# Kernel tuning notes

Hardware: AMD Instinct MI355X
Metric: run time of the kernel (lower is better)

## Reference

```python
import jax, jax.numpy as jnp
import numpy as np

NIN = 4096
NOUT = 4096
LN_EPS = 1e-5  # torch.nn.LayerNorm default


def setup_inputs() -> dict:
    key = jax.random.key(0)
    ks = jax.random.split(key, 8)
    x = jax.random.normal(ks[0], (1, NIN), dtype=jnp.float32)
    hid = jax.random.normal(ks[1], (1, NOUT), dtype=jnp.float32)
    hebb = jnp.zeros((NOUT, NOUT), dtype=jnp.float32) + 1e-6  # initialZeroHebb
    # parameters
    w_in = 0.01 * jax.random.normal(ks[2], (NOUT, NIN), dtype=jnp.float32)  # inp_lin weight (no bias)
    w = 0.01 * jnp.eye(NOUT, NOUT, dtype=jnp.float32)                        # Plastic.w
    alpha = 0.01 * jax.random.normal(ks[3], (NOUT, NOUT), dtype=jnp.float32)
    b = 0.01 * jax.random.normal(ks[4], (NOUT,), dtype=jnp.float32)
    lamda = 0.01 * jnp.ones((1,), dtype=jnp.float32)
    pred_eta = 0.01 * jax.random.normal(ks[5], (NOUT, NOUT), dtype=jnp.float32)
    pred_eta_b = 0.01 * jax.random.normal(ks[6], (NOUT,), dtype=jnp.float32)
    ln_gamma = jnp.ones((NOUT,), dtype=jnp.float32)
    ln_beta = jnp.zeros((NOUT,), dtype=jnp.float32)
    return {"x": x, "hid": hid, "hebb": hebb, "w_in": w_in, "w": w,
            "alpha": alpha, "b": b, "lamda": lamda, "pred_eta": pred_eta,
            "pred_eta_b": pred_eta_b, "ln_gamma": ln_gamma, "ln_beta": ln_beta}


def reference(x, hid, hebb, w_in, w, alpha, b, lamda, pred_eta, pred_eta_b, ln_gamma, ln_beta):
    # Cell.forward (nonlin = ReLU for both wx and the post-LN output)
    wx = jax.nn.relu(x @ w_in.T)                       # [1, nout]
    wh = hid @ (w + alpha * hebb) + b                  # Plastic.forward, [1, nout]
    s = wx + wh
    mu = jnp.mean(s, axis=-1, keepdims=True)
    var = jnp.mean((s - mu) ** 2, axis=-1, keepdims=True)
    ln = ln_gamma * (s - mu) * jax.lax.rsqrt(var + LN_EPS) + ln_beta
    wy = jax.nn.relu(ln)                               # new hidden state, [1, nout]
    # Plastic.update_hebb(x=hid, y=wh, hebb)
    eta_hat = jax.nn.sigmoid(wh @ pred_eta + pred_eta_b)           # [1, nout]
    outer = hid[0, :, None] * wh[0, None, :]                        # [nout, nout]
    hebb_new = (1.0 - lamda) * hebb + eta_hat.T * outer             # row i scaled by eta_hat[0, i]
    return wy, hebb_new
```

## Files before the change

### kernel.cpp

```cpp
#include <hip/hip_runtime.h>
#include <hip/hip_bf16.h>
#include <math.h>

#define N 4096
#define NGRP 16

typedef float f32x4 __attribute__((ext_vector_type(4)));

__inline__ __device__ float waveReduceSum(float v) {
    #pragma unroll
    for (int o = 32; o > 0; o >>= 1) v += __shfl_down(v, o);
    return v;
}

#define LD4(p, o) (*reinterpret_cast<const float4*>((p) + (o)))

__inline__ __device__ f32x4 ntld4(const float* p) {
    return __builtin_nontemporal_load(reinterpret_cast<const f32x4*>(p));
}

template<int ITERS>
__global__ __launch_bounds__(256) void k_sweep_wh_t(const float* __restrict__ hid,
                                                    const float* __restrict__ w,
                                                    const float* __restrict__ alpha,
                                                    const float* __restrict__ hebb,
                                                    float* __restrict__ part,
                                                    int G) {
    int b = blockIdx.x, t = threadIdx.x;
    int p = b >> 2;
    int j0 = (((b & 3) << 8) | t) * 4;
    int P = G >> 2;
    size_t step = (size_t)G * 1024;
    size_t off = (size_t)(((b << 8) | t)) * 4;

    f32x4 wv[ITERS], av[ITERS], bv[ITERS];
    float hv[ITERS];
    #pragma unroll
    for (int k = 0; k < ITERS; ++k) {
        size_t o = off + (size_t)k * step;
        wv[k] = ntld4(w + o);
        av[k] = ntld4(alpha + o);
        bv[k] = *reinterpret_cast<const f32x4*>(hebb + o);
    }
    #pragma unroll
    for (int k = 0; k < ITERS; ++k) hv[k] = hid[k * P + p];

    f32x4 acc = {0.f, 0.f, 0.f, 0.f};
    #pragma unroll
    for (int k = 0; k < ITERS; ++k) {
        float h = hv[k];
        acc.x = fmaf(h, fmaf(av[k].x, bv[k].x, wv[k].x), acc.x);
        acc.y = fmaf(h, fmaf(av[k].y, bv[k].y, wv[k].y), acc.y);
        acc.z = fmaf(h, fmaf(av[k].z, bv[k].z, wv[k].z), acc.z);
        acc.w = fmaf(h, fmaf(av[k].w, bv[k].w, wv[k].w), acc.w);
    }
    *reinterpret_cast<f32x4*>(part + (size_t)p * N + j0) = acc;
}

__global__ __launch_bounds__(256) void k_sweep_wh(const float* __restrict__ hid,
                                                  const float* __restrict__ w,
                                                  const float* __restrict__ alpha,
                                                  const float* __restrict__ hebb,
                                                  float* __restrict__ part,
                                                  int G, int iters) {
    int b = blockIdx.x, t = threadIdx.x;
    int p = b >> 2;
    int j0 = (((b & 3) << 8) | t) * 4;
    int P = G >> 2;
    float4 acc = make_float4(0.f, 0.f, 0.f, 0.f);
    size_t step = (size_t)G * 1024;
    size_t off = (size_t)(((b << 8) | t)) * 4;
    #pragma unroll 8
    for (int k = 0; k < iters; ++k, off += step) {
        float h = hid[k * P + p];
        float4 wv = LD4(w, off);
        float4 av = LD4(alpha, off);
        float4 hv = LD4(hebb, off);
        acc.x = fmaf(h, fmaf(av.x, hv.x, wv.x), acc.x);
        acc.y = fmaf(h, fmaf(av.y, hv.y, wv.y), acc.y);
        acc.z = fmaf(h, fmaf(av.z, hv.z, wv.z), acc.z);
        acc.w = fmaf(h, fmaf(av.w, hv.w, wv.w), acc.w);
    }
    *reinterpret_cast<float4*>(part + (size_t)p * N + j0) = acc;
}

template<int ITERS>
__global__ __launch_bounds__(256) void k_sweep_eta_t(const float* __restrict__ wh,
                                                     const float* __restrict__ pe,
                                                     float* __restrict__ part,
                                                     int G) {
    int b = blockIdx.x, t = threadIdx.x;
    int p = b >> 2;
    int j0 = (((b & 3) << 8) | t) * 4;
    int P = G >> 2;
    size_t step = (size_t)G * 1024;
    size_t off = (size_t)(((b << 8) | t)) * 4;

    f32x4 pv[ITERS];
    float hv[ITERS];
    #pragma unroll
    for (int k = 0; k < ITERS; ++k) pv[k] = *reinterpret_cast<const f32x4*>(pe + off + (size_t)k * step);
    #pragma unroll
    for (int k = 0; k < ITERS; ++k) hv[k] = wh[k * P + p];

    f32x4 acc = {0.f, 0.f, 0.f, 0.f};
    #pragma unroll
    for (int k = 0; k < ITERS; ++k) {
        float h = hv[k];
        acc.x = fmaf(h, pv[k].x, acc.x);
        acc.y = fmaf(h, pv[k].y, acc.y);
        acc.z = fmaf(h, pv[k].z, acc.z);
        acc.w = fmaf(h, pv[k].w, acc.w);
    }
    *reinterpret_cast<f32x4*>(part + (size_t)p * N + j0) = acc;
}

__global__ __launch_bounds__(256) void k_sweep_eta(const float* __restrict__ wh,
                                                   const float* __restrict__ pe,
                                                   float* __restrict__ part,
                                                   int G, int iters) {
    int b = blockIdx.x, t = threadIdx.x;
    int p = b >> 2;
    int j0 = (((b & 3) << 8) | t) * 4;
    int P = G >> 2;
    float4 acc = make_float4(0.f, 0.f, 0.f, 0.f);
    size_t step = (size_t)G * 1024;
    size_t off = (size_t)(((b << 8) | t)) * 4;
    #pragma unroll 8
    for (int k = 0; k < iters; ++k, off += step) {
        float h = wh[k * P + p];
        float4 pv = LD4(pe, off);
        acc.x = fmaf(h, pv.x, acc.x);
        acc.y = fmaf(h, pv.y, acc.y);
        acc.z = fmaf(h, pv.z, acc.z);
        acc.w = fmaf(h, pv.w, acc.w);
    }
    *reinterpret_cast<float4*>(part + (size_t)p * N + j0) = acc;
}

__global__ __launch_bounds__(256) void k_red_wx(const float* __restrict__ part,
                                                float* __restrict__ part2,
                                                int cpg,
                                                const float* __restrict__ x,
                                                const float* __restrict__ w_in,
                                                float* __restrict__ wx_out,
                                                int nred) {
    int t = threadIdx.x;
    if ((int)blockIdx.x < nred) {
        int g  = blockIdx.x >> 2;
        int xt = blockIdx.x & 3;
        int j0 = (xt * 256 + t) * 4;
        const float4* p4 = reinterpret_cast<const float4*>(part);
        float4 s = make_float4(0.f, 0.f, 0.f, 0.f);
        #pragma unroll 8
        for (int c = 0; c < cpg; ++c) {
            float4 v = p4[((size_t)(g * cpg + c) * N + j0) >> 2];
            s.x += v.x; s.y += v.y; s.z += v.z; s.w += v.w;
        }
        *reinterpret_cast<float4*>(part2 + (size_t)g * N + j0) = s;
    } else {
        int j = blockIdx.x - nred;
        const float4* row = reinterpret_cast<const float4*>(w_in + (size_t)j * N);
        const float4* xv  = reinterpret_cast<const float4*>(x);
        float sum = 0.f;
        #pragma unroll
        for (int k = t; k < N / 4; k += 256) {
            float4 a = row[k], c = xv[k];
            sum += a.x * c.x + a.y * c.y + a.z * c.z + a.w * c.w;
        }
        sum = waveReduceSum(sum);
        __shared__ float wsum[4];
        int wid = t >> 6, lane = t & 63;
        if (lane == 0) wsum[wid] = sum;
        __syncthreads();
        if (t == 0)
            wx_out[j] = fmaxf(wsum[0] + wsum[1] + wsum[2] + wsum[3], 0.f);
    }
}

__global__ __launch_bounds__(1024) void k_ln(const float* __restrict__ part2,
                                             const float* __restrict__ wx,
                                             const float* __restrict__ b,
                                             const float* __restrict__ gamma,
                                             const float* __restrict__ beta,
                                             float* __restrict__ wh_out,
                                             float* __restrict__ wy_out) {
    __shared__ float red[16];
    __shared__ float bc[2];
    int tid = threadIdx.x;
    int wid = tid >> 6, lane = tid & 63;
    float sv[4];
    float lsum = 0.f;
    #pragma unroll
    for (int q = 0; q < 4; ++q) {
        int j = q * 1024 + tid;
        float acc = b[j];
        #pragma unroll
        for (int g = 0; g < NGRP; ++g) acc += part2[(size_t)g * N + j];
        wh_out[j] = acc;
        float s = acc + wx[j];
        sv[q] = s;
        lsum += s;
    }
    float wv = waveReduceSum(lsum);
    if (lane == 0) red[wid] = wv;
    __syncthreads();
    if (tid < 64) {
        float t = (tid < 16) ? red[tid] : 0.f;
        t = waveReduceSum(t);
        if (tid == 0) bc[0] = t * (1.f / N);
    }
    __syncthreads();
    float mean = bc[0];
    __syncthreads();
    float lsq = 0.f;
    #pragma unroll
    for (int q = 0; q < 4; ++q) { float d = sv[q] - mean; lsq += d * d; }
    wv = waveReduceSum(lsq);
    if (lane == 0) red[wid] = wv;
    __syncthreads();
    if (tid < 64) {
        float t = (tid < 16) ? red[tid] : 0.f;
        t = waveReduceSum(t);
        if (tid == 0) bc[1] = t * (1.f / N);
    }
    __syncthreads();
    float rstd = rsqrtf(bc[1] + 1e-5f);
    #pragma unroll
    for (int q = 0; q < 4; ++q) {
        int j = q * 1024 + tid;
        float ln = fmaf(gamma[j] * (sv[q] - mean), rstd, beta[j]);
        wy_out[j] = fmaxf(ln, 0.f);
    }
}

__global__ __launch_bounds__(1024) void k_redfin_hebb(const float* __restrict__ part,
                                                      const float* __restrict__ pb,
                                                      const float* __restrict__ wh,
                                                      const float* __restrict__ hid,
                                                      const float* __restrict__ lamda,
                                                      const float* __restrict__ hebb,
                                                      float* __restrict__ out,
                                                      int P) {
    __shared__ float sm[64][17];
    __shared__ float coef_s[16];
    int t  = threadIdx.x;
    int i0 = blockIdx.x * 16;
    int il = t & 15;
    int ps = t >> 4;
    int q  = P >> 6;

    float s = 0.f;
    for (int k = 0; k < q; ++k)
        s += part[(size_t)(ps * q + k) * N + i0 + il];
    sm[ps][il] = s;
    __syncthreads();
    #pragma unroll
    for (int off = 32; off >= 1; off >>= 1) {
        if (ps < off) sm[ps][il] += sm[ps + off][il];
        __syncthreads();
    }
    if (t < 16) {
        int i = i0 + t;
        float eta = 1.f / (1.f + expf(-(sm[0][t] + pb[i])));
        coef_s[t] = eta * hid[i];
    }
    __syncthreads();

    float decay = 1.f - lamda[0];
    int j = t * 4;
    float4 w4 = LD4(wh, j);
    size_t base = (size_t)i0 * N + j;
    #pragma unroll 4
    for (int r = 0; r < 16; ++r) {
        float coef = coef_s[r];
        float4 h = LD4(hebb, base + (size_t)r * N);
        f32x4 o;
        o.x = fmaf(decay, h.x, coef * w4.x);
        o.y = fmaf(decay, h.y, coef * w4.y);
        o.z = fmaf(decay, h.z, coef * w4.z);
        o.w = fmaf(decay, h.w, coef * w4.w);
        __builtin_nontemporal_store(o, reinterpret_cast<f32x4*>(out + base + (size_t)r * N));
    }
}

extern "C" void kernel_launch(void* const* d_in, const int* in_sizes, int n_in,
                              void* d_out, int out_size, void* d_ws, size_t ws_size,
                              hipStream_t stream) {
    const float* x         = (const float*)d_in[0];
    const float* hid       = (const float*)d_in[1];
    const float* hebb      = (const float*)d_in[2];
    const float* w_in      = (const float*)d_in[3];
    const float* w         = (const float*)d_in[4];
    const float* alpha     = (const float*)d_in[5];
    const float* b         = (const float*)d_in[6];
    const float* lamda     = (const float*)d_in[7];
    const float* pred_eta  = (const float*)d_in[8];
    const float* pred_eta_b= (const float*)d_in[9];
    const float* ln_gamma  = (const float*)d_in[10];
    const float* ln_beta   = (const float*)d_in[11];

    float* wy       = (float*)d_out;
    float* hebb_out = (float*)d_out + N;

    int G = 2048;
    if ((ws_size / 4) < ((size_t)(G / 4) * N + (NGRP + 2) * (size_t)N)) G = 512;
    int P = G / 4;
    int cpg = P / NGRP;
    int iters = (N * (N / 4)) / (G * 256);
    int nred = 4 * NGRP;

    float* ws    = (float*)d_ws;
    float* part  = ws;
    float* part2 = part + (size_t)P * N;
    float* wx    = part2 + (size_t)NGRP * N;
    float* wh    = wx + N;

    if (G == 2048) {
        k_sweep_wh_t<8><<<G, 256, 0, stream>>>(hid, w, alpha, hebb, part, G);
    } else {
        k_sweep_wh<<<G, 256, 0, stream>>>(hid, w, alpha, hebb, part, G, iters);
    }
    k_red_wx<<<nred + N, 256, 0, stream>>>(part, part2, cpg, x, w_in, wx, nred);
    k_ln    <<<1, 1024, 0, stream>>>(part2, wx, b, ln_gamma, ln_beta, wh, wy);
    if (G == 2048) {
        k_sweep_eta_t<8><<<G, 256, 0, stream>>>(wh, pred_eta, part, G);
    } else {
        k_sweep_eta<<<G, 256, 0, stream>>>(wh, pred_eta, part, G, iters);
    }
    k_redfin_hebb<<<256, 1024, 0, stream>>>(part, pred_eta_b, wh, hid, lamda, hebb, hebb_out, P);
}
```

Before: 97.28 us.

## Fuse five-kernel pipeline into one cooperative persistent kernel with grid syncs

Replaces the five-launch sequence (wh sweep, reduce+wx, layernorm, eta sweep, reduce+hebb update) with a single cooperative kernel of 1024 blocks that separates phases with grid.sync(). The wx GEMV is folded into the first phase, and the final reduction now writes per-row coefficients before a separate hebb update phase. This is meant to remove launch gaps and inter-kernel drains. In exchange it adds grid-wide barriers, halves the grid size so each block sweeps 16 rows, and runs the layernorm serially on a single block while the rest of the grid waits. It falls back to the old path if cooperative launch is unavailable or occupancy is too low, and the fallback drops the small-workspace G=512 variant.

```diff
diff --git a/kernel.cpp b/kernel.cpp
--- a/kernel.cpp
+++ b/kernel.cpp
@@ -1,10 +1,13 @@
 #include <hip/hip_runtime.h>
+#include <hip/hip_cooperative_groups.h>
 #include <hip/hip_bf16.h>
 #include <math.h>
 
 #define N 4096
 #define NGRP 16
 
+namespace cg = cooperative_groups;
+
 typedef float f32x4 __attribute__((ext_vector_type(4)));
 
 __inline__ __device__ float waveReduceSum(float v) {
@@ -17,6 +20,207 @@
 
 __inline__ __device__ f32x4 ntld4(const float* p) {
     return __builtin_nontemporal_load(reinterpret_cast<const f32x4*>(p));
+}
+
+template<int ITERS>
+__global__ __launch_bounds__(256, 4) void k_coop(
+    const float* __restrict__ x, const float* __restrict__ hid,
+    const float* __restrict__ hebb, const float* __restrict__ w_in,
+    const float* __restrict__ w, const float* __restrict__ alpha,
+    const float* __restrict__ bvec, const float* __restrict__ lamda,
+    const float* __restrict__ pe, const float* __restrict__ pb,
+    const float* __restrict__ gamma, const float* __restrict__ beta,
+    float* __restrict__ part, float* __restrict__ part2,
+    float* __restrict__ wxv, float* __restrict__ whv,
+    float* __restrict__ coef, float* __restrict__ wy,
+    float* __restrict__ hebb_out, int G)
+{
+    cg::grid_group grid = cg::this_grid();
+    const int b = blockIdx.x, t = threadIdx.x;
+    const int P = G >> 2;
+    const int lane = t & 63, wid = t >> 6;
+    __shared__ float sm[16][17];
+    __shared__ float smb[4];
+    __shared__ float bc[2];
+
+    {
+        int p = b >> 2;
+        int j0 = (((b & 3) << 8) | t) * 4;
+        size_t step = (size_t)G * 1024;
+        size_t off = (size_t)(((b << 8) | t)) * 4;
+        f32x4 acc = {0.f, 0.f, 0.f, 0.f};
+        #pragma unroll
+        for (int h8 = 0; h8 < ITERS / 8; ++h8) {
+            f32x4 wv[8], av[8], bv[8];
+            float hv[8];
+            #pragma unroll
+            for (int k = 0; k < 8; ++k) {
+                size_t o = off + (size_t)(h8 * 8 + k) * step;
+                wv[k] = ntld4(w + o);
+                av[k] = ntld4(alpha + o);
+                bv[k] = *reinterpret_cast<const f32x4*>(hebb + o);
+            }
+            #pragma unroll
+            for (int k = 0; k < 8; ++k) hv[k] = hid[(h8 * 8 + k) * P + p];
+            #pragma unroll
+            for (int k = 0; k < 8; ++k) {
+                float h = hv[k];
+                acc.x = fmaf(h, fmaf(av[k].x, bv[k].x, wv[k].x), acc.x);
+                acc.y = fmaf(h, fmaf(av[k].y, bv[k].y, wv[k].y), acc.y);
+                acc.z = fmaf(h, fmaf(av[k].z, bv[k].z, wv[k].z), acc.z);
+                acc.w = fmaf(h, fmaf(av[k].w, bv[k].w, wv[k].w), acc.w);
+            }
+        }
+        *reinterpret_cast<f32x4*>(part + (size_t)p * N + j0) = acc;
+    }
+    {
+        int rpb = N / G;
+        const float4* xv = reinterpret_cast<const float4*>(x);
+        for (int r = 0; r < rpb; ++r) {
+            int j = b * rpb + r;
+            const float4* row = reinterpret_cast<const float4*>(w_in + (size_t)j * N);
+            float sum = 0.f;
+            #pragma unroll
+            for (int c = 0; c < 4; ++c) {
+                int k = t + c * 256;
+                float4 a = row[k], xc = xv[k];
+                sum += a.x * xc.x + a.y * xc.y + a.z * xc.z + a.w * xc.w;
+            }
+            sum = waveReduceSum(sum);
+            if (lane == 0) smb[wid] = sum;
+            __syncthreads();
+            if (t == 0) wxv[j] = fmaxf(smb[0] + smb[1] + smb[2] + smb[3], 0.f);
+            __syncthreads();
+        }
+    }
+    grid.sync();
+
+    if (b < 4 * NGRP) {
+        int g = b >> 2, xt = b & 3;
+        int j0 = (xt * 256 + t) * 4;
+        int cpg = P / NGRP;
+        const f32x4* p4 = reinterpret_cast<const f32x4*>(part);
+        f32x4 s = {0.f, 0.f, 0.f, 0.f};
+        for (int c = 0; c < cpg; ++c) {
+            f32x4 v = p4[((size_t)(g * cpg + c) * N + j0) >> 2];
+            s.x += v.x; s.y += v.y; s.z += v.z; s.w += v.w;
+        }
+        *reinterpret_cast<f32x4*>(part2 + (size_t)g * N + j0) = s;
+    }
+    grid.sync();
+
+    if (b == 0) {
+        float sv[16];
+        float lsum = 0.f;
+        #pragma unroll
+        for (int q = 0; q < 16; ++q) {
+            int j = q * 256 + t;
+            float acc = bvec[j];
+            #pragma unroll
+            for (int g = 0; g < NGRP; ++g) acc += part2[(size_t)g * N + j];
+            whv[j] = acc;
+            float s = acc + wxv[j];
+            sv[q] = s;
+            lsum += s;
+        }
+        float wr = waveReduceSum(lsum);
+        if (lane == 0) smb[wid] = wr;
+        __syncthreads();
+        if (t == 0) bc[0] = (smb[0] + smb[1] + smb[2] + smb[3]) * (1.f / N);
+        __syncthreads();
+        float mean = bc[0];
+        float lsq = 0.f;
+        #pragma unroll
+        for (int q = 0; q < 16; ++q) { float d = sv[q] - mean; lsq += d * d; }
+        float wr2 = waveReduceSum(lsq);
+        if (lane == 0) smb[wid] = wr2;
+        __syncthreads();
+        if (t == 0) bc[1] = (smb[0] + smb[1] + smb[2] + smb[3]) * (1.f / N);
+        __syncthreads();
+        float rstd = rsqrtf(bc[1] + 1e-5f);
+        #pragma unroll
+        for (int q = 0; q < 16; ++q) {
+            int j = q * 256 + t;
+            float ln = fmaf(gamma[j] * (sv[q] - mean), rstd, beta[j]);
+            wy[j] = fmaxf(ln, 0.f);
+        }
+    }
+    grid.sync();
+
+    {
+        int p = b >> 2;
+        int j0 = (((b & 3) << 8) | t) * 4;
+        size_t step = (size_t)G * 1024;
+        size_t off = (size_t)(((b << 8) | t)) * 4;
+        f32x4 acc = {0.f, 0.f, 0.f, 0.f};
+        #pragma unroll
+        for (int h8 = 0; h8 < ITERS / 8; ++h8) {
+            f32x4 pv[8];
+            float hv[8];
+            #pragma unroll
+            for (int k = 0; k < 8; ++k)
+                pv[k] = *reinterpret_cast<const f32x4*>(pe + off + (size_t)(h8 * 8 + k) * step);
+            #pragma unroll
+            for (int k = 0; k < 8; ++k) hv[k] = whv[(h8 * 8 + k) * P + p];
+            #pragma unroll
+            for (int k = 0; k < 8; ++k) {
+                float h = hv[k];
+                acc.x = fmaf(h, pv[k].x, acc.x);
+                acc.y = fmaf(h, pv[k].y, acc.y);
+                acc.z = fmaf(h, pv[k].z, acc.z);
+                acc.w = fmaf(h, pv[k].w, acc.w);
+            }
+        }
+        *reinterpret_cast<f32x4*>(part + (size_t)p * N + j0) = acc;
+    }
+    grid.sync();
+
+    if (b < 256) {
+        int i0 = b * 16;
+        int il = t & 15, ps = t >> 4;
+        int q2 = P >> 4;
+        float s = 0.f;
+        for (int k = 0; k < q2; ++k)
+            s += part[(size_t)(ps * q2 + k) * N + i0 + il];
+        sm[ps][il] = s;
+        __syncthreads();
+        #pragma unroll
+        for (int off2 = 8; off2 >= 1; off2 >>= 1) {
+            if (ps < off2) sm[ps][il] += sm[ps + off2][il];
+            __syncthreads();
+        }
+        if (t < 16) {
+            int i = i0 + t;
+            float eta = 1.f / (1.f + expf(-(sm[0][t] + pb[i])));
+            coef[i] = eta * hid[i];
+        }
+    }
+    grid.sync();
+
+    {
+        float decay = 1.f - lamda[0];
+        int rpb = N / G;
+        for (int r = 0; r < rpb; ++r) {
+            int i = b * rpb + r;
+            float cf = coef[i];
+            size_t base = (size_t)i * N;
+            const f32x4* hrow = reinterpret_cast<const f32x4*>(hebb + base);
+            f32x4* orow = reinterpret_cast<f32x4*>(hebb_out + base);
+            const f32x4* wrow = reinterpret_cast<const f32x4*>(whv);
+            #pragma unroll
+            for (int c = 0; c < 4; ++c) {
+                int k = t + c * 256;
+                f32x4 h = hrow[k];
+                f32x4 wv4 = wrow[k];
+                f32x4 o;
+                o.x = fmaf(decay, h.x, cf * wv4.x);
+                o.y = fmaf(decay, h.y, cf * wv4.y);
+                o.z = fmaf(decay, h.z, cf * wv4.z);
+                o.w = fmaf(decay, h.w, cf * wv4.w);
+                __builtin_nontemporal_store(o, orow + k);
+            }
+        }
+    }
 }
 
 template<int ITERS>
@@ -32,7 +236,6 @@
     int P = G >> 2;
     size_t step = (size_t)G * 1024;
     size_t off = (size_t)(((b << 8) | t)) * 4;
-
     f32x4 wv[ITERS], av[ITERS], bv[ITERS];
     float hv[ITERS];
     #pragma unroll
@@ -44,7 +247,6 @@
     }
     #pragma unroll
     for (int k = 0; k < ITERS; ++k) hv[k] = hid[k * P + p];
-
     f32x4 acc = {0.f, 0.f, 0.f, 0.f};
     #pragma unroll
     for (int k = 0; k < ITERS; ++k) {
@@ -55,33 +257,6 @@
         acc.w = fmaf(h, fmaf(av[k].w, bv[k].w, wv[k].w), acc.w);
     }
     *reinterpret_cast<f32x4*>(part + (size_t)p * N + j0) = acc;
-}
-
-__global__ __launch_bounds__(256) void k_sweep_wh(const float* __restrict__ hid,
-                                                  const float* __restrict__ w,
-                                                  const float* __restrict__ alpha,
-                                                  const float* __restrict__ hebb,
-                                                  float* __restrict__ part,
-                                                  int G, int iters) {
-    int b = blockIdx.x, t = threadIdx.x;
-    int p = b >> 2;
-    int j0 = (((b & 3) << 8) | t) * 4;
-    int P = G >> 2;
-    float4 acc = make_float4(0.f, 0.f, 0.f, 0.f);
-    size_t step = (size_t)G * 1024;
-    size_t off = (size_t)(((b << 8) | t)) * 4;
-    #pragma unroll 8
-    for (int k = 0; k < iters; ++k, off += step) {
-        float h = hid[k * P + p];
-        float4 wv = LD4(w, off);
-        float4 av = LD4(alpha, off);
-        float4 hv = LD4(hebb, off);
-        acc.x = fmaf(h, fmaf(av.x, hv.x, wv.x), acc.x);
-        acc.y = fmaf(h, fmaf(av.y, hv.y, wv.y), acc.y);
-        acc.z = fmaf(h, fmaf(av.z, hv.z, wv.z), acc.z);
-        acc.w = fmaf(h, fmaf(av.w, hv.w, wv.w), acc.w);
-    }
-    *reinterpret_cast<float4*>(part + (size_t)p * N + j0) = acc;
 }
 
 template<int ITERS>
@@ -95,14 +270,12 @@
     int P = G >> 2;
     size_t step = (size_t)G * 1024;
     size_t off = (size_t)(((b << 8) | t)) * 4;
-
     f32x4 pv[ITERS];
     float hv[ITERS];
     #pragma unroll
     for (int k = 0; k < ITERS; ++k) pv[k] = *reinterpret_cast<const f32x4*>(pe + off + (size_t)k * step);
     #pragma unroll
     for (int k = 0; k < ITERS; ++k) hv[k] = wh[k * P + p];
-
     f32x4 acc = {0.f, 0.f, 0.f, 0.f};
     #pragma unroll
     for (int k = 0; k < ITERS; ++k) {
@@ -113,29 +286,6 @@
         acc.w = fmaf(h, pv[k].w, acc.w);
     }
     *reinterpret_cast<f32x4*>(part + (size_t)p * N + j0) = acc;
-}
-
-__global__ __launch_bounds__(256) void k_sweep_eta(const float* __restrict__ wh,
-                                                   const float* __restrict__ pe,
-                                                   float* __restrict__ part,
-                                                   int G, int iters) {
-    int b = blockIdx.x, t = threadIdx.x;
-    int p = b >> 2;
-    int j0 = (((b & 3) << 8) | t) * 4;
-    int P = G >> 2;
-    float4 acc = make_float4(0.f, 0.f, 0.f, 0.f);
-    size_t step = (size_t)G * 1024;
-    size_t off = (size_t)(((b << 8) | t)) * 4;
-    #pragma unroll 8
-    for (int k = 0; k < iters; ++k, off += step) {
-        float h = wh[k * P + p];
-        float4 pv = LD4(pe, off);
-        acc.x = fmaf(h, pv.x, acc.x);
-        acc.y = fmaf(h, pv.y, acc.y);
-        acc.z = fmaf(h, pv.z, acc.z);
-        acc.w = fmaf(h, pv.w, acc.w);
-    }
-    *reinterpret_cast<float4*>(part + (size_t)p * N + j0) = acc;
 }
 
 __global__ __launch_bounds__(256) void k_red_wx(const float* __restrict__ part,
@@ -293,7 +443,7 @@
     const float* w_in      = (const float*)d_in[3];
     const float* w         = (const float*)d_in[4];
     const float* alpha     = (const float*)d_in[5];
-    const float* b         = (const float*)d_in[6];
+    const float* bvec      = (const float*)d_in[6];
     const float* lamda     = (const float*)d_in[7];
     const float* pred_eta  = (const float*)d_in[8];
     const float* pred_eta_b= (const float*)d_in[9];
@@ -303,30 +453,52 @@
     float* wy       = (float*)d_out;
     float* hebb_out = (float*)d_out + N;
 
+    const int Gc = 1024;
+    const int Pc = Gc / 4;
+    bool wsOK = (ws_size / 4) >= ((size_t)Pc * N + (size_t)(NGRP + 3) * N);
+
+    int dev = 0;
+    hipGetDevice(&dev);
+    int coopAttr = 0, numCU = 0;
+    hipDeviceGetAttribute(&coopAttr, hipDeviceAttributeCooperativeLaunch, dev);
+    hipDeviceGetAttribute(&numCU, hipDeviceAttributeMultiprocessorCount, dev);
+    int maxB = 0;
+    hipOccupancyMaxActiveBlocksPerMultiprocessor(&maxB, (const void*)&k_coop<16>, 256, 0);
+
+    if (coopAttr && wsOK && maxB > 0 && (size_t)maxB * (size_t)numCU >= (size_t)Gc) {
+        float* ws    = (float*)d_ws;
+        float* part  = ws;
+        float* part2 = part + (size_t)Pc * N;
+        float* wxv   = part2 + (size_t)NGRP * N;
+        float* whv   = wxv + N;
+        float* coef  = whv + N;
+        int Gl = Gc;
+        void* args[] = {
+            (void*)&x, (void*)&hid, (void*)&hebb, (void*)&w_in, (void*)&w,
+            (void*)&alpha, (void*)&bvec, (void*)&lamda, (void*)&pred_eta,
+            (void*)&pred_eta_b, (void*)&ln_gamma, (void*)&ln_beta,
+            (void*)&part, (void*)&part2, (void*)&wxv, (void*)&whv,
+            (void*)&coef, (void*)&wy, (void*)&hebb_out, (void*)&Gl
+        };
+        hipError_t err = hipLaunchCooperativeKernel((const void*)&k_coop<16>,
+                                                    dim3(Gc), dim3(256), args, 0, stream);
+        if (err == hipSuccess) return;
+    }
+
     int G = 2048;
-    if ((ws_size / 4) < ((size_t)(G / 4) * N + (NGRP + 2) * (size_t)N)) G = 512;
     int P = G / 4;
     int cpg = P / NGRP;
-    int iters = (N * (N / 4)) / (G * 256);
     int nred = 4 * NGRP;
 
     float* ws    = (float*)d_ws;
     float* part  = ws;
     float* part2 = part + (size_t)P * N;
-    float* wx    = part2 + (size_t)NGRP * N;
-    float* wh    = wx + N;
-
-    if (G == 2048) {
-        k_sweep_wh_t<8><<<G, 256, 0, stream>>>(hid, w, alpha, hebb, part, G);
-    } else {
-        k_sweep_wh<<<G, 256, 0, stream>>>(hid, w, alpha, hebb, part, G, iters);
-    }
-    k_red_wx<<<nred + N, 256, 0, stream>>>(part, part2, cpg, x, w_in, wx, nred);
-    k_ln    <<<1, 1024, 0, stream>>>(part2, wx, b, ln_gamma, ln_beta, wh, wy);
-    if (G == 2048) {
-        k_sweep_eta_t<8><<<G, 256, 0, stream>>>(wh, pred_eta, part, G);
-    } else {
-        k_sweep_eta<<<G, 256, 0, stream>>>(wh, pred_eta, part, G, iters);
-    }
-    k_redfin_hebb<<<256, 1024, 0, stream>>>(part, pred_eta_b, wh, hid, lamda, hebb, hebb_out, P);
-}
+    float* wxv   = part2 + (size_t)NGRP * N;
+    float* whv   = wxv + N;
+
+    k_sweep_wh_t<8><<<G, 256, 0, stream>>>(hid, w, alpha, hebb, part, G);
+    k_red_wx<<<nred + N, 256, 0, stream>>>(part, part2, cpg, x, w_in, wxv, nred);
+    k_ln    <<<1, 1024, 0, stream>>>(part2, wxv, bvec, ln_gamma, ln_beta, whv, wy);
+    k_sweep_eta_t<8><<<G, 256, 0, stream>>>(whv, pred_eta, part, G);
+    k_redfin_hebb<<<256, 1024, 0, stream>>>(part, pred_eta_b, whv, hid, lamda, hebb, hebb_out, P);
+}
```

Result: no change. 96.03 us (-1.3%).
